# Kernel tuning notes

Measured on AMD Instinct MI355X. Metric: run time of the kernel, lower is better.

The kernel has to match this reference:

```python
import jax, jax.numpy as jnp
import numpy as np

N_NODES = 100000
N_EDGES = 1600000
IN_DIM = 128
HID = 128
EMB = 64


def _glorot(key, shape):
    fan_in, fan_out = shape[0], shape[1]
    lim = np.sqrt(6.0 / (fan_in + fan_out))
    return jax.random.uniform(key, shape, jnp.float32, -lim, lim)


def setup_inputs() -> dict:
    key = jax.random.key(0)
    ks = jax.random.split(key, 16)
    x = jax.random.normal(ks[0], (N_NODES, IN_DIM), jnp.float32)
    src = jax.random.randint(ks[1], (N_EDGES,), 0, N_NODES, jnp.int64)
    dst = jax.random.randint(ks[2], (N_EDGES,), 0, N_NODES, jnp.int64)
    # GCN encoder weights (GraphConv: weight [in,out], bias [out])
    W1 = _glorot(ks[3], (IN_DIM, HID)); b1 = jnp.zeros((HID,), jnp.float32)
    W2 = _glorot(ks[4], (HID, EMB)); b2 = jnp.zeros((EMB,), jnp.float32)
    # MLP predictor: 2*EMB=128 -> 64 -> 32 -> 1
    Wp1 = _glorot(ks[5], (2 * EMB, 64)); bp1 = jnp.zeros((64,), jnp.float32)
    Wp2 = _glorot(ks[6], (64, 32)); bp2 = jnp.zeros((32,), jnp.float32)
    Wp3 = _glorot(ks[7], (32, 1)); bp3 = jnp.zeros((1,), jnp.float32)
    return {"x": x, "src": src, "dst": dst,
            "W1": W1, "b1": b1, "W2": W2, "b2": b2,
            "Wp1": Wp1, "bp1": bp1, "Wp2": Wp2, "bp2": bp2,
            "Wp3": Wp3, "bp3": bp3}


def _gcn_conv(x, src, dst, W, b, n_nodes):
    # DGL GraphConv, norm='both': symmetric degree normalization, sum aggregation.
    ones = jnp.ones((src.shape[0],), x.dtype)
    deg_out = jnp.clip(jax.ops.segment_sum(ones, src, num_segments=n_nodes), 1.0)
    deg_in = jnp.clip(jax.ops.segment_sum(ones, dst, num_segments=n_nodes), 1.0)
    h = (x * jax.lax.rsqrt(deg_out)[:, None]) @ W          # [N, out]
    agg = jax.ops.segment_sum(h[src], dst, num_segments=n_nodes)  # gather + scatter-add
    return agg * jax.lax.rsqrt(deg_in)[:, None] + b


def reference(x, src, dst, W1, b1, W2, b2, Wp1, bp1, Wp2, bp2, Wp3, bp3):
    n = x.shape[0]
    h = jax.nn.relu(_gcn_conv(x, src, dst, W1, b1, n))   # layer 1 (with activation)
    h = _gcn_conv(h, src, dst, W2, b2, n)                # layer 2 (no activation)
    # edge-wise concat of endpoint embeddings: [E, 2*EMB]
    emb = jnp.concatenate([h[src], h[dst]], axis=1)
    z = jax.nn.relu(emb @ Wp1 + bp1)
    z = jax.nn.relu(z @ Wp2 + bp2)
    score = z @ Wp3 + bp3                                # [E, 1]
    return jax.nn.sigmoid(score)
```

## Files before the change

kernel.cpp:

```cpp
#include <hip/hip_runtime.h>
#include <math.h>


#define NBLK 256
#define NBUK 512
#define GRD (NBUK * NBLK)
#define GRT (2 * GRD)

typedef __attribute__((ext_vector_type(8))) short bf16x8;
typedef __attribute__((ext_vector_type(4))) float f32x4;

__device__ __forceinline__ float bl(unsigned u) { return __uint_as_float(u << 16); }
__device__ __forceinline__ float bh(unsigned u) { return __uint_as_float(u & 0xffff0000u); }
__device__ __forceinline__ unsigned short f2bf(float f) {
  unsigned u = __float_as_uint(f);
  return (unsigned short)((u + 0x7fffu + ((u >> 16) & 1u)) >> 16);
}
__device__ __forceinline__ unsigned packbf2(float a, float b) {
  return (unsigned)f2bf(a) | ((unsigned)f2bf(b) << 16);
}


__global__ __launch_bounds__(256) void k_hist(
    const int* __restrict__ src, const int* __restrict__ dst,
    int* __restrict__ grams, int E,
    const float* __restrict__ W1, const float* __restrict__ W2,
    const float* __restrict__ Wp1, const float* __restrict__ Wp2,
    unsigned short* __restrict__ W1t, unsigned short* __restrict__ W2t,
    unsigned short* __restrict__ Wct, unsigned short* __restrict__ Wp2t) {
  __shared__ int hd[NBUK], hs[NBUK];
  int blk = blockIdx.x, t = threadIdx.x;
  {
    int i = blk * 256 + t;
    if (i < 16384) {
      int n = i >> 7, k = i & 127;
      W1t[i] = f2bf(W1[k * 128 + n]);
    } else if (i < 24576) {
      int j = i - 16384; int n = j >> 7, k = j & 127;
      W2t[j] = f2bf(W2[k * 64 + n]);
    } else if (i < 32768) {
      int j = i - 24576; int c = j >> 6, k = j & 63;
      float v = (c < 64) ? Wp1[k * 64 + c] : Wp1[(k + 64) * 64 + (c - 64)];
      Wct[j] = f2bf(v);
    } else if (i < 34816) {
      int j = i - 32768; int n = j >> 6, k = j & 63;
      Wp2t[j] = f2bf(Wp2[k * 32 + n]);
    }
  }
  for (int k = t; k < NBUK; k += 256) { hd[k] = 0; hs[k] = 0; }
  __syncthreads();
  int chunk = (E + NBLK - 1) / NBLK;
  int start = blk * chunk, end = min(E, start + chunk);
  for (int i = start + t; i < end; i += 256) {
    atomicAdd(&hd[dst[i] >> 8], 1);
    atomicAdd(&hs[src[i] >> 8], 1);
  }
  __syncthreads();
  for (int k = t; k < NBUK; k += 256) {
    grams[k * NBLK + blk] = hd[k];
    grams[GRD + k * NBLK + blk] = hs[k];
  }
}

__global__ __launch_bounds__(256) void k_gscan1(const int* __restrict__ g,
                                                int* __restrict__ bsum) {
  __shared__ int lds[256];
  int b = blockIdx.x, t = threadIdx.x;
  int base = b * 1024 + t * 4;
  int s = g[base] + g[base + 1] + g[base + 2] + g[base + 3];
  lds[t] = s; __syncthreads();
  for (int st = 128; st > 0; st >>= 1) {
    if (t < st) lds[t] += lds[t + st];
    __syncthreads();
  }
  if (t == 0) bsum[b] = lds[0];
}

__global__ __launch_bounds__(256) void k_gscan3(int* __restrict__ g,
                                                const int* __restrict__ bsum) {
  __shared__ int lds[256], lds2[256];
  int b = blockIdx.x, t = threadIdx.x;
  int bv = bsum[t];
  lds2[t] = bv; __syncthreads();
  for (int st = 1; st < 256; st <<= 1) {
    int add = (t >= st) ? lds2[t - st] : 0;
    __syncthreads();
    lds2[t] += add;
    __syncthreads();
  }
  int bpref = (b > 0) ? lds2[b - 1] : 0;

  int base = b * 1024 + t * 4;
  int v[4]; int s = 0;
#pragma unroll
  for (int j = 0; j < 4; j++) { v[j] = g[base + j]; s += v[j]; }
  lds[t] = s; __syncthreads();
  int mine = s;
  for (int st = 1; st < 256; st <<= 1) {
    int add = (t >= st) ? lds[t - st] : 0;
    __syncthreads();
    lds[t] += add;
    __syncthreads();
  }
  int excl = lds[t] - mine + bpref;
#pragma unroll
  for (int j = 0; j < 4; j++) { g[base + j] = excl; excl += v[j]; }
}

__global__ __launch_bounds__(256) void k_part(
    const int* __restrict__ src, const int* __restrict__ dst,
    const int* __restrict__ grams, uint2* __restrict__ pdst,
    int* __restrict__ sbuf, int E) {
  __shared__ int curd[NBUK], curs[NBUK];
  int blk = blockIdx.x, t = threadIdx.x;
  for (int k = t; k < NBUK; k += 256) {
    curd[k] = grams[k * NBLK + blk];
    curs[k] = grams[GRD + k * NBLK + blk] - E;
  }
  __syncthreads();
  int chunk = (E + NBLK - 1) / NBLK;
  int start = blk * chunk, end = min(E, start + chunk);
  for (int i = start + t; i < end; i += 256) {
    int s = src[i], d = dst[i];
    int pd = atomicAdd(&curd[d >> 8], 1);
    pdst[pd] = make_uint2((unsigned)s, (unsigned)i | ((unsigned)(d & 255) << 21));
    int ps = atomicAdd(&curs[s >> 8], 1);
    sbuf[ps] = s;
  }
}

__global__ __launch_bounds__(256) void k_dcsr(
    const uint2* __restrict__ pdst, const int* __restrict__ sbuf,
    const int* __restrict__ grams,
    int* __restrict__ adj, int* __restrict__ dnode, int* __restrict__ eidx,
    int* __restrict__ rowst, float* __restrict__ rin, float* __restrict__ rout,
    int N, int E) {
  __shared__ int hist[256], cur[256];
  int b = blockIdx.x, t = threadIdx.x;
  int base = grams[b * 256];
  int end  = grams[b * 256 + 256];
  hist[t] = 0; __syncthreads();
  for (int i = base + t; i < end; i += 256)
    atomicAdd(&hist[(pdst[i].y >> 21) & 255], 1);
  __syncthreads();
  int cnt = hist[t];
  for (int st = 1; st < 256; st <<= 1) {
    int add = (t >= st) ? hist[t - st] : 0;
    __syncthreads();
    hist[t] += add;
    __syncthreads();
  }
  int excl = hist[t] - cnt;
  cur[t] = excl;
  int node = b * 256 + t;
  if (node < N) {
    rowst[node] = base + excl;
    rin[node] = rsqrtf((float)max(cnt, 1));
  }
  __syncthreads();
  for (int i = base + t; i < end; i += 256) {
    uint2 u = pdst[i];
    int lo = (u.y >> 21) & 255;
    int eid = (int)(u.y & 0x1FFFFFu);
    int pos = base + atomicAdd(&cur[lo], 1);
    adj[pos] = (int)u.x;
    dnode[pos] = b * 256 + lo;
    eidx[pos] = eid;
  }
  __syncthreads();
  hist[t] = 0; __syncthreads();
  int sb = grams[GRD + b * 256] - E;
  int se = grams[GRD + b * 256 + 256] - E;
  for (int i = sb + t; i < se; i += 256)
    atomicAdd(&hist[sbuf[i] & 255], 1);
  __syncthreads();
  if (node < N) rout[node] = rsqrtf((float)max(hist[t], 1));
}

template <int K, int BN, bool ABF, bool SC>
__global__ __launch_bounds__(256) void k_gemm(
    const void* __restrict__ Av, const float* __restrict__ scale,
    const unsigned short* __restrict__ Wt, unsigned short* __restrict__ C, int M) {
  constexpr int KP = K + 8;
  __shared__ __attribute__((aligned(16))) unsigned short As[64][KP];
  __shared__ __attribute__((aligned(16))) unsigned short Ws[BN][KP];
  int tid = threadIdx.x;
  int row0 = blockIdx.x * 64;

  for (int i = tid; i < BN * K / 8; i += 256) {
    int n = i / (K / 8), seg = i % (K / 8);
    *(uint4*)&Ws[n][seg * 8] = ((const uint4*)Wt)[i];
  }
  {
    constexpr int CH = K / 4;
    int r = tid >> 2, q = tid & 3;
    int row = row0 + r;
    if (row < M) {
      float sc = SC ? scale[row] : 1.0f;
      if constexpr (!ABF) {
        const float4* ap = (const float4*)((const float*)Av + (size_t)row * K + q * CH);
#pragma unroll
        for (int c = 0; c < CH / 8; c++) {
          float4 v0 = ap[2 * c], v1 = ap[2 * c + 1];
          uint4 o;
          o.x = packbf2(v0.x * sc, v0.y * sc);
          o.y = packbf2(v0.z * sc, v0.w * sc);
          o.z = packbf2(v1.x * sc, v1.y * sc);
          o.w = packbf2(v1.z * sc, v1.w * sc);
          *(uint4*)&As[r][q * CH + c * 8] = o;
        }
      } else {
        const uint4* ap = (const uint4*)((const unsigned short*)Av + (size_t)row * K + q * CH);
#pragma unroll
        for (int c = 0; c < CH / 8; c++) {
          uint4 v = ap[c];
          if constexpr (SC) {
            uint4 o;
            o.x = packbf2(bl(v.x) * sc, bh(v.x) * sc);
            o.y = packbf2(bl(v.y) * sc, bh(v.y) * sc);
            o.z = packbf2(bl(v.z) * sc, bh(v.z) * sc);
            o.w = packbf2(bl(v.w) * sc, bh(v.w) * sc);
            *(uint4*)&As[r][q * CH + c * 8] = o;
          } else {
            *(uint4*)&As[r][q * CH + c * 8] = v;
          }
        }
      }
    } else {
#pragma unroll
      for (int c = 0; c < CH / 8; c++)
        *(uint4*)&As[r][q * CH + c * 8] = make_uint4(0, 0, 0, 0);
    }
  }
  __syncthreads();

  constexpr int KS = K / 32;
  constexpr int NT = BN / 16;
  int wav = tid >> 6, lane = tid & 63;
  int quad = lane >> 4, lrow = lane & 15;
  int mb = wav * 16;

  bf16x8 af[KS];
#pragma unroll
  for (int s = 0; s < KS; s++)
    af[s] = *(const bf16x8*)&As[mb + lrow][s * 32 + quad * 8];

  f32x4 acc[NT];
#pragma unroll
  for (int nt = 0; nt < NT; nt++) acc[nt] = (f32x4){0.f, 0.f, 0.f, 0.f};
#pragma unroll
  for (int nt = 0; nt < NT; nt++) {
#pragma unroll
    for (int s = 0; s < KS; s++) {
      bf16x8 bf = *(const bf16x8*)&Ws[nt * 16 + lrow][s * 32 + quad * 8];
      acc[nt] = __builtin_amdgcn_mfma_f32_16x16x32_bf16(af[s], bf, acc[nt], 0, 0, 0);
    }
  }
#pragma unroll
  for (int nt = 0; nt < NT; nt++) {
#pragma unroll
    for (int reg = 0; reg < 4; reg++) {
      int row = row0 + mb + quad * 4 + reg;
      if (row < M) C[(size_t)row * BN + nt * 16 + lrow] = f2bf(acc[nt][reg]);
    }
  }
}

template <int F>
__global__ __launch_bounds__(256) void k_agg(
    const unsigned short* __restrict__ hin, const int* __restrict__ rowst,
    const int* __restrict__ adj, const float* __restrict__ rin,
    const float* __restrict__ bias, unsigned short* __restrict__ hout,
    int N, int E, int do_relu) {
  int node = (blockIdx.x * 256 + threadIdx.x) >> 6;
  int lane = threadIdx.x & 63;
  if (node >= N) return;
  int start = rowst[node];
  int end = (node + 1 < N) ? rowst[node + 1] : E;
  int half = lane >> 5, fl = lane & 31;
  if (F == 128) {
    const uint2* h2 = (const uint2*)hin;
    float a0 = 0.f, a1 = 0.f, a2 = 0.f, a3 = 0.f;
    float c0 = 0.f, c1 = 0.f, c2 = 0.f, c3 = 0.f;
    int i = start + half;
    for (; i + 2 < end; i += 4) {
      uint2 w0 = h2[(size_t)adj[i] * 32 + fl];
      uint2 w1 = h2[(size_t)adj[i + 2] * 32 + fl];
      a0 += bl(w0.x); a1 += bh(w0.x); a2 += bl(w0.y); a3 += bh(w0.y);
      c0 += bl(w1.x); c1 += bh(w1.x); c2 += bl(w1.y); c3 += bh(w1.y);
    }
    if (i < end) {
      uint2 w0 = h2[(size_t)adj[i] * 32 + fl];
      a0 += bl(w0.x); a1 += bh(w0.x); a2 += bl(w0.y); a3 += bh(w0.y);
    }
    a0 += c0; a1 += c1; a2 += c2; a3 += c3;
    a0 += __shfl_xor(a0, 32, 64);
    a1 += __shfl_xor(a1, 32, 64);
    a2 += __shfl_xor(a2, 32, 64);
    a3 += __shfl_xor(a3, 32, 64);
    float r = rin[node];
    float o0 = fmaf(a0, r, bias[fl * 4 + 0]);
    float o1 = fmaf(a1, r, bias[fl * 4 + 1]);
    float o2 = fmaf(a2, r, bias[fl * 4 + 2]);
    float o3 = fmaf(a3, r, bias[fl * 4 + 3]);
    if (do_relu) {
      o0 = fmaxf(o0, 0.f); o1 = fmaxf(o1, 0.f);
      o2 = fmaxf(o2, 0.f); o3 = fmaxf(o3, 0.f);
    }
    if (half == 0) {
      uint2 o; o.x = packbf2(o0, o1); o.y = packbf2(o2, o3);
      *(uint2*)((unsigned*)hout + (size_t)node * 64 + fl * 2) = o;
    }
  } else {
    const unsigned* h2 = (const unsigned*)hin;
    float a0 = 0.f, a1 = 0.f, c0 = 0.f, c1 = 0.f;
    int i = start + half;
    for (; i + 2 < end; i += 4) {
      unsigned w0 = h2[(size_t)adj[i] * 32 + fl];
      unsigned w1 = h2[(size_t)adj[i + 2] * 32 + fl];
      a0 += bl(w0); a1 += bh(w0);
      c0 += bl(w1); c1 += bh(w1);
    }
    if (i < end) {
      unsigned w0 = h2[(size_t)adj[i] * 32 + fl];
      a0 += bl(w0); a1 += bh(w0);
    }
    a0 += c0; a1 += c1;
    a0 += __shfl_xor(a0, 32, 64);
    a1 += __shfl_xor(a1, 32, 64);
    float r = rin[node];
    float o0 = fmaf(a0, r, bias[fl * 2 + 0]);
    float o1 = fmaf(a1, r, bias[fl * 2 + 1]);
    if (do_relu) { o0 = fmaxf(o0, 0.f); o1 = fmaxf(o1, 0.f); }
    if (half == 0)
      ((unsigned*)hout)[(size_t)node * 32 + fl] = packbf2(o0, o1);
  }
}

__global__ __launch_bounds__(256) void k_edge(
    const unsigned short* __restrict__ ab, const int* __restrict__ adj,
    const int* __restrict__ dnode, const int* __restrict__ eidx,
    const unsigned short* __restrict__ Wp2t, const float* __restrict__ bp1,
    const float* __restrict__ bp2, const float* __restrict__ Wp3,
    const float* __restrict__ bp3, float* __restrict__ out, int E) {
  __shared__ __attribute__((aligned(16))) unsigned short z1s[128][72];
  __shared__ __attribute__((aligned(16))) unsigned short w2t[32][72];
  __shared__ float sb1[64], sb2[32], sw3[32];

  int t = threadIdx.x;
  {
    uint4 v = ((const uint4*)Wp2t)[t];
    int n = t >> 3, seg = t & 7;
    *(uint4*)&w2t[n][seg * 8] = v;
    if (t < 64) sb1[t] = bp1[t];
    else if (t < 96) sb2[t - 64] = bp2[t - 64];
    else if (t < 128) sw3[t - 96] = Wp3[t - 96];
  }
  __syncthreads();

  int p0 = blockIdx.x * 128;
  {
    int m = t >> 1, half = t & 1, p = p0 + m;
    int s = 0, d = 0;
    if (p < E) { s = adj[p]; d = dnode[p]; }
    const uint4* apf = (const uint4*)(ab + (size_t)s * 128 + half * 32);
    const uint4* bpf = (const uint4*)(ab + (size_t)d * 128 + 64 + half * 32);
    int jb = half * 32;
#pragma unroll
    for (int q = 0; q < 4; q++) {
      uint4 av = apf[q], bv = bpf[q];
      int j = jb + 8 * q;
      float z0 = fmaxf(bl(av.x) + bl(bv.x) + sb1[j + 0], 0.f);
      float z1 = fmaxf(bh(av.x) + bh(bv.x) + sb1[j + 1], 0.f);
      float z2 = fmaxf(bl(av.y) + bl(bv.y) + sb1[j + 2], 0.f);
      float z3 = fmaxf(bh(av.y) + bh(bv.y) + sb1[j + 3], 0.f);
      float z4 = fmaxf(bl(av.z) + bl(bv.z) + sb1[j + 4], 0.f);
      float z5 = fmaxf(bh(av.z) + bh(bv.z) + sb1[j + 5], 0.f);
      float z6 = fmaxf(bl(av.w) + bl(bv.w) + sb1[j + 6], 0.f);
      float z7 = fmaxf(bh(av.w) + bh(bv.w) + sb1[j + 7], 0.f);
      uint4 o;
      o.x = packbf2(z0, z1); o.y = packbf2(z2, z3);
      o.z = packbf2(z4, z5); o.w = packbf2(z6, z7);
      *(uint4*)&z1s[m][j] = o;
    }
  }
  __syncthreads();

  int wav = t >> 6, lane = t & 63;
  int quad = lane >> 4, lrow = lane & 15;

  bf16x8 bfr[2][2];
#pragma unroll
  for (int s = 0; s < 2; s++)
#pragma unroll
    for (int nt = 0; nt < 2; nt++)
      bfr[s][nt] = *(const bf16x8*)&w2t[nt * 16 + lrow][s * 32 + quad * 8];

  f32x4 acc[2][2];
#pragma unroll
  for (int mt = 0; mt < 2; mt++)
#pragma unroll
    for (int nt = 0; nt < 2; nt++) acc[mt][nt] = (f32x4){0.f, 0.f, 0.f, 0.f};

#pragma unroll
  for (int mt = 0; mt < 2; mt++) {
    int mb = (wav * 2 + mt) * 16;
#pragma unroll
    for (int s = 0; s < 2; s++) {
      bf16x8 a = *(const bf16x8*)&z1s[mb + lrow][s * 32 + quad * 8];
#pragma unroll
      for (int nt = 0; nt < 2; nt++)
        acc[mt][nt] = __builtin_amdgcn_mfma_f32_16x16x32_bf16(a, bfr[s][nt], acc[mt][nt], 0, 0, 0);
    }
  }

  float bb0 = sb2[lrow], bb1 = sb2[16 + lrow];
  float w30 = sw3[lrow], w31 = sw3[16 + lrow];
  float p2[2][4];
#pragma unroll
  for (int mt = 0; mt < 2; mt++)
#pragma unroll
    for (int reg = 0; reg < 4; reg++)
      p2[mt][reg] = fmaxf(acc[mt][0][reg] + bb0, 0.f) * w30 +
                    fmaxf(acc[mt][1][reg] + bb1, 0.f) * w31;
#pragma unroll
  for (int off = 1; off < 16; off <<= 1) {
#pragma unroll
    for (int mt = 0; mt < 2; mt++)
#pragma unroll
      for (int reg = 0; reg < 4; reg++)
        p2[mt][reg] += __shfl_xor(p2[mt][reg], off, 64);
  }
  if (lrow < 4) {
    float b3 = bp3[0];
#pragma unroll
    for (int mt = 0; mt < 2; mt++) {
      float score = p2[mt][0];
      if (lrow == 1) score = p2[mt][1];
      if (lrow == 2) score = p2[mt][2];
      if (lrow == 3) score = p2[mt][3];
      score += b3;
      int pp = p0 + (wav * 2 + mt) * 16 + quad * 4 + lrow;
      if (pp < E) out[eidx[pp]] = 1.0f / (1.0f + __expf(-score));
    }
  }
}

extern "C" void kernel_launch(void* const* d_in, const int* in_sizes, int n_in,
                              void* d_out, int out_size, void* d_ws, size_t ws_size,
                              hipStream_t stream) {
  const float* x   = (const float*)d_in[0];
  const int*   src = (const int*)d_in[1];
  const int*   dst = (const int*)d_in[2];
  const float* W1  = (const float*)d_in[3];
  const float* b1  = (const float*)d_in[4];
  const float* W2  = (const float*)d_in[5];
  const float* b2  = (const float*)d_in[6];
  const float* Wp1 = (const float*)d_in[7];
  const float* bp1 = (const float*)d_in[8];
  const float* Wp2 = (const float*)d_in[9];
  const float* bp2 = (const float*)d_in[10];
  const float* Wp3 = (const float*)d_in[11];
  const float* bp3 = (const float*)d_in[12];
  float* out = (float*)d_out;

  int N = in_sizes[0] / 128;
  int E = in_sizes[1];

  char* w = (char*)d_ws;
  unsigned short* bufA = (unsigned short*)w;
  uint2* pdst = (uint2*)w;
  int*   sbuf = (int*)(w + (size_t)E * 8);
  w += (size_t)N * 128 * 2;
  unsigned short* bufB = (unsigned short*)w; w += (size_t)N * 128 * 2;
  int* grams  = (int*)w;    w += (size_t)GRT * sizeof(int);
  int* bsum   = (int*)w;    w += 256 * sizeof(int);
  int* rowst  = (int*)w;    w += (size_t)N * sizeof(int);
  int* adj    = (int*)w;    w += (size_t)E * sizeof(int);
  int* dnode  = (int*)w;    w += (size_t)E * sizeof(int);
  int* eidx   = (int*)w;    w += (size_t)E * sizeof(int);
  float* rin  = (float*)w;  w += (size_t)N * sizeof(float);
  float* rout = (float*)w;  w += (size_t)N * sizeof(float);
  unsigned short* W1t  = (unsigned short*)w; w += 16384 * 2;
  unsigned short* W2t  = (unsigned short*)w; w += 8192 * 2;
  unsigned short* Wct  = (unsigned short*)w; w += 8192 * 2;
  unsigned short* Wp2t = (unsigned short*)w; w += 2048 * 2;

  int nbk = (N + 255) / 256;

  k_hist<<<NBLK, 256, 0, stream>>>(src, dst, grams, E, W1, W2, Wp1, Wp2,
                                   W1t, W2t, Wct, Wp2t);
  k_gscan1<<<GRT / 1024, 256, 0, stream>>>(grams, bsum);
  k_gscan3<<<GRT / 1024, 256, 0, stream>>>(grams, bsum);
  k_part<<<NBLK, 256, 0, stream>>>(src, dst, grams, pdst, sbuf, E);
  k_dcsr<<<nbk, 256, 0, stream>>>(pdst, sbuf, grams, adj, dnode, eidx,
                                  rowst, rin, rout, N, E);

  k_gemm<128, 128, false, true><<<(N + 63) / 64, 256, 0, stream>>>(x, rout, W1t, bufA, N);
  k_agg<128><<<(N + 3) / 4, 256, 0, stream>>>(bufA, rowst, adj, rin, b1, bufB, N, E, 1);
  k_gemm<128, 64, true, true><<<(N + 63) / 64, 256, 0, stream>>>(bufB, rout, W2t, bufA, N);
  k_agg<64><<<(N + 3) / 4, 256, 0, stream>>>(bufA, rowst, adj, rin, b2, bufB, N, E, 0);
  k_gemm<64, 128, true, false><<<(N + 63) / 64, 256, 0, stream>>>(bufB, nullptr, Wct, bufA, N);
  k_edge<<<(E + 127) / 128, 256, 0, stream>>>(bufA, adj, dnode, eidx, Wp2t,
                                              bp1, bp2, Wp3, bp3, out, E);
}
```

Baseline: 433.3 us.

## Compact CSR build, process edges in original order, widen agg gather to 16B

The partition buffer is packed from 8 bytes to 4 bytes per edge, and the source histogram buffer now stores a single low byte. The dnode and eidx arrays are dropped, so the edge MLP reads src and dst directly in original order and writes output without a scatter. The aggregation kernel now gives each thread 16-byte vector loads, with 16 or 8 threads per node and four neighbors unrolled per step, replacing half-wave splitting and shuffles. This cuts memory traffic in CSR construction and the edge stage, at the cost of losing the dst-sorted locality the edge kernel previously had when gathering embeddings.

```diff
diff --git a/kernel.cpp b/kernel.cpp
--- a/kernel.cpp
+++ b/kernel.cpp
@@ -109,8 +109,8 @@
 
 __global__ __launch_bounds__(256) void k_part(
     const int* __restrict__ src, const int* __restrict__ dst,
-    const int* __restrict__ grams, uint2* __restrict__ pdst,
-    int* __restrict__ sbuf, int E) {
+    const int* __restrict__ grams, unsigned* __restrict__ pdst,
+    unsigned char* __restrict__ sbuf, int E) {
   __shared__ int curd[NBUK], curs[NBUK];
   int blk = blockIdx.x, t = threadIdx.x;
   for (int k = t; k < NBUK; k += 256) {
@@ -123,25 +123,24 @@
   for (int i = start + t; i < end; i += 256) {
     int s = src[i], d = dst[i];
     int pd = atomicAdd(&curd[d >> 8], 1);
-    pdst[pd] = make_uint2((unsigned)s, (unsigned)i | ((unsigned)(d & 255) << 21));
+    pdst[pd] = ((unsigned)s << 8) | (unsigned)(d & 255);
     int ps = atomicAdd(&curs[s >> 8], 1);
-    sbuf[ps] = s;
+    sbuf[ps] = (unsigned char)(s & 255);
   }
 }
 
 __global__ __launch_bounds__(256) void k_dcsr(
-    const uint2* __restrict__ pdst, const int* __restrict__ sbuf,
+    const unsigned* __restrict__ pdst, const unsigned char* __restrict__ sbuf,
     const int* __restrict__ grams,
-    int* __restrict__ adj, int* __restrict__ dnode, int* __restrict__ eidx,
-    int* __restrict__ rowst, float* __restrict__ rin, float* __restrict__ rout,
-    int N, int E) {
+    int* __restrict__ adj, int* __restrict__ rowst,
+    float* __restrict__ rin, float* __restrict__ rout, int N, int E) {
   __shared__ int hist[256], cur[256];
   int b = blockIdx.x, t = threadIdx.x;
   int base = grams[b * 256];
   int end  = grams[b * 256 + 256];
   hist[t] = 0; __syncthreads();
   for (int i = base + t; i < end; i += 256)
-    atomicAdd(&hist[(pdst[i].y >> 21) & 255], 1);
+    atomicAdd(&hist[pdst[i] & 255], 1);
   __syncthreads();
   int cnt = hist[t];
   for (int st = 1; st < 256; st <<= 1) {
@@ -159,20 +158,16 @@
   }
   __syncthreads();
   for (int i = base + t; i < end; i += 256) {
-    uint2 u = pdst[i];
-    int lo = (u.y >> 21) & 255;
-    int eid = (int)(u.y & 0x1FFFFFu);
-    int pos = base + atomicAdd(&cur[lo], 1);
-    adj[pos] = (int)u.x;
-    dnode[pos] = b * 256 + lo;
-    eidx[pos] = eid;
+    unsigned u = pdst[i];
+    int pos = base + atomicAdd(&cur[u & 255], 1);
+    adj[pos] = (int)(u >> 8);
   }
   __syncthreads();
   hist[t] = 0; __syncthreads();
   int sb = grams[GRD + b * 256] - E;
   int se = grams[GRD + b * 256 + 256] - E;
   for (int i = sb + t; i < se; i += 256)
-    atomicAdd(&hist[sbuf[i] & 255], 1);
+    atomicAdd(&hist[sbuf[i]], 1);
   __syncthreads();
   if (node < N) rout[node] = rsqrtf((float)max(hist[t], 1));
 }
@@ -272,74 +267,64 @@
     const int* __restrict__ adj, const float* __restrict__ rin,
     const float* __restrict__ bias, unsigned short* __restrict__ hout,
     int N, int E, int do_relu) {
-  int node = (blockIdx.x * 256 + threadIdx.x) >> 6;
-  int lane = threadIdx.x & 63;
+  constexpr int TPN = F / 8;
+  constexpr int NPB = 256 / TPN;
+  int node = blockIdx.x * NPB + threadIdx.x / TPN;
+  int c = threadIdx.x % TPN;
   if (node >= N) return;
   int start = rowst[node];
   int end = (node + 1 < N) ? rowst[node + 1] : E;
-  int half = lane >> 5, fl = lane & 31;
-  if (F == 128) {
-    const uint2* h2 = (const uint2*)hin;
-    float a0 = 0.f, a1 = 0.f, a2 = 0.f, a3 = 0.f;
-    float c0 = 0.f, c1 = 0.f, c2 = 0.f, c3 = 0.f;
-    int i = start + half;
-    for (; i + 2 < end; i += 4) {
-      uint2 w0 = h2[(size_t)adj[i] * 32 + fl];
-      uint2 w1 = h2[(size_t)adj[i + 2] * 32 + fl];
-      a0 += bl(w0.x); a1 += bh(w0.x); a2 += bl(w0.y); a3 += bh(w0.y);
-      c0 += bl(w1.x); c1 += bh(w1.x); c2 += bl(w1.y); c3 += bh(w1.y);
-    }
-    if (i < end) {
-      uint2 w0 = h2[(size_t)adj[i] * 32 + fl];
-      a0 += bl(w0.x); a1 += bh(w0.x); a2 += bl(w0.y); a3 += bh(w0.y);
-    }
-    a0 += c0; a1 += c1; a2 += c2; a3 += c3;
-    a0 += __shfl_xor(a0, 32, 64);
-    a1 += __shfl_xor(a1, 32, 64);
-    a2 += __shfl_xor(a2, 32, 64);
-    a3 += __shfl_xor(a3, 32, 64);
-    float r = rin[node];
-    float o0 = fmaf(a0, r, bias[fl * 4 + 0]);
-    float o1 = fmaf(a1, r, bias[fl * 4 + 1]);
-    float o2 = fmaf(a2, r, bias[fl * 4 + 2]);
-    float o3 = fmaf(a3, r, bias[fl * 4 + 3]);
-    if (do_relu) {
-      o0 = fmaxf(o0, 0.f); o1 = fmaxf(o1, 0.f);
-      o2 = fmaxf(o2, 0.f); o3 = fmaxf(o3, 0.f);
-    }
-    if (half == 0) {
-      uint2 o; o.x = packbf2(o0, o1); o.y = packbf2(o2, o3);
-      *(uint2*)((unsigned*)hout + (size_t)node * 64 + fl * 2) = o;
-    }
-  } else {
-    const unsigned* h2 = (const unsigned*)hin;
-    float a0 = 0.f, a1 = 0.f, c0 = 0.f, c1 = 0.f;
-    int i = start + half;
-    for (; i + 2 < end; i += 4) {
-      unsigned w0 = h2[(size_t)adj[i] * 32 + fl];
-      unsigned w1 = h2[(size_t)adj[i + 2] * 32 + fl];
-      a0 += bl(w0); a1 += bh(w0);
-      c0 += bl(w1); c1 += bh(w1);
-    }
-    if (i < end) {
-      unsigned w0 = h2[(size_t)adj[i] * 32 + fl];
-      a0 += bl(w0); a1 += bh(w0);
-    }
-    a0 += c0; a1 += c1;
-    a0 += __shfl_xor(a0, 32, 64);
-    a1 += __shfl_xor(a1, 32, 64);
-    float r = rin[node];
-    float o0 = fmaf(a0, r, bias[fl * 2 + 0]);
-    float o1 = fmaf(a1, r, bias[fl * 2 + 1]);
-    if (do_relu) { o0 = fmaxf(o0, 0.f); o1 = fmaxf(o1, 0.f); }
-    if (half == 0)
-      ((unsigned*)hout)[(size_t)node * 32 + fl] = packbf2(o0, o1);
-  }
+  const uint4* h4 = (const uint4*)hin;
+
+  float a[8], b[8];
+#pragma unroll
+  for (int j = 0; j < 8; j++) { a[j] = 0.f; b[j] = 0.f; }
+
+  int i = start;
+  for (; i + 3 < end; i += 4) {
+    uint4 w0 = h4[(size_t)adj[i] * TPN + c];
+    uint4 w1 = h4[(size_t)adj[i + 1] * TPN + c];
+    uint4 w2 = h4[(size_t)adj[i + 2] * TPN + c];
+    uint4 w3 = h4[(size_t)adj[i + 3] * TPN + c];
+    a[0] += bl(w0.x); a[1] += bh(w0.x); a[2] += bl(w0.y); a[3] += bh(w0.y);
+    a[4] += bl(w0.z); a[5] += bh(w0.z); a[6] += bl(w0.w); a[7] += bh(w0.w);
+    b[0] += bl(w1.x); b[1] += bh(w1.x); b[2] += bl(w1.y); b[3] += bh(w1.y);
+    b[4] += bl(w1.z); b[5] += bh(w1.z); b[6] += bl(w1.w); b[7] += bh(w1.w);
+    a[0] += bl(w2.x); a[1] += bh(w2.x); a[2] += bl(w2.y); a[3] += bh(w2.y);
+    a[4] += bl(w2.z); a[5] += bh(w2.z); a[6] += bl(w2.w); a[7] += bh(w2.w);
+    b[0] += bl(w3.x); b[1] += bh(w3.x); b[2] += bl(w3.y); b[3] += bh(w3.y);
+    b[4] += bl(w3.z); b[5] += bh(w3.z); b[6] += bl(w3.w); b[7] += bh(w3.w);
+  }
+  for (; i < end; i++) {
+    uint4 w0 = h4[(size_t)adj[i] * TPN + c];
+    a[0] += bl(w0.x); a[1] += bh(w0.x); a[2] += bl(w0.y); a[3] += bh(w0.y);
+    a[4] += bl(w0.z); a[5] += bh(w0.z); a[6] += bl(w0.w); a[7] += bh(w0.w);
+  }
+  float r = rin[node];
+  const float4* bp = (const float4*)(bias + c * 8);
+  float4 bb0 = bp[0], bb1 = bp[1];
+  float o0 = fmaf(a[0] + b[0], r, bb0.x);
+  float o1 = fmaf(a[1] + b[1], r, bb0.y);
+  float o2 = fmaf(a[2] + b[2], r, bb0.z);
+  float o3 = fmaf(a[3] + b[3], r, bb0.w);
+  float o4 = fmaf(a[4] + b[4], r, bb1.x);
+  float o5 = fmaf(a[5] + b[5], r, bb1.y);
+  float o6 = fmaf(a[6] + b[6], r, bb1.z);
+  float o7 = fmaf(a[7] + b[7], r, bb1.w);
+  if (do_relu) {
+    o0 = fmaxf(o0, 0.f); o1 = fmaxf(o1, 0.f); o2 = fmaxf(o2, 0.f);
+    o3 = fmaxf(o3, 0.f); o4 = fmaxf(o4, 0.f); o5 = fmaxf(o5, 0.f);
+    o6 = fmaxf(o6, 0.f); o7 = fmaxf(o7, 0.f);
+  }
+  uint4 o;
+  o.x = packbf2(o0, o1); o.y = packbf2(o2, o3);
+  o.z = packbf2(o4, o5); o.w = packbf2(o6, o7);
+  ((uint4*)hout)[(size_t)node * TPN + c] = o;
 }
 
 __global__ __launch_bounds__(256) void k_edge(
-    const unsigned short* __restrict__ ab, const int* __restrict__ adj,
-    const int* __restrict__ dnode, const int* __restrict__ eidx,
+    const unsigned short* __restrict__ ab, const int* __restrict__ src,
+    const int* __restrict__ dst,
     const unsigned short* __restrict__ Wp2t, const float* __restrict__ bp1,
     const float* __restrict__ bp2, const float* __restrict__ Wp3,
     const float* __restrict__ bp3, float* __restrict__ out, int E) {
@@ -362,7 +347,7 @@
   {
     int m = t >> 1, half = t & 1, p = p0 + m;
     int s = 0, d = 0;
-    if (p < E) { s = adj[p]; d = dnode[p]; }
+    if (p < E) { s = src[p]; d = dst[p]; }
     const uint4* apf = (const uint4*)(ab + (size_t)s * 128 + half * 32);
     const uint4* bpf = (const uint4*)(ab + (size_t)d * 128 + 64 + half * 32);
     int jb = half * 32;
@@ -441,7 +426,7 @@
       if (lrow == 3) score = p2[mt][3];
       score += b3;
       int pp = p0 + (wav * 2 + mt) * 16 + quad * 4 + lrow;
-      if (pp < E) out[eidx[pp]] = 1.0f / (1.0f + __expf(-score));
+      if (pp < E) out[pp] = 1.0f / (1.0f + __expf(-score));
     }
   }
 }
@@ -469,16 +454,14 @@
 
   char* w = (char*)d_ws;
   unsigned short* bufA = (unsigned short*)w;
-  uint2* pdst = (uint2*)w;
-  int*   sbuf = (int*)(w + (size_t)E * 8);
+  unsigned* pdst = (unsigned*)w;
+  unsigned char* sbuf = (unsigned char*)(w + (size_t)E * 4);
   w += (size_t)N * 128 * 2;
   unsigned short* bufB = (unsigned short*)w; w += (size_t)N * 128 * 2;
   int* grams  = (int*)w;    w += (size_t)GRT * sizeof(int);
   int* bsum   = (int*)w;    w += 256 * sizeof(int);
   int* rowst  = (int*)w;    w += (size_t)N * sizeof(int);
   int* adj    = (int*)w;    w += (size_t)E * sizeof(int);
-  int* dnode  = (int*)w;    w += (size_t)E * sizeof(int);
-  int* eidx   = (int*)w;    w += (size_t)E * sizeof(int);
   float* rin  = (float*)w;  w += (size_t)N * sizeof(float);
   float* rout = (float*)w;  w += (size_t)N * sizeof(float);
   unsigned short* W1t  = (unsigned short*)w; w += 16384 * 2;
@@ -493,14 +476,13 @@
   k_gscan1<<<GRT / 1024, 256, 0, stream>>>(grams, bsum);
   k_gscan3<<<GRT / 1024, 256, 0, stream>>>(grams, bsum);
   k_part<<<NBLK, 256, 0, stream>>>(src, dst, grams, pdst, sbuf, E);
-  k_dcsr<<<nbk, 256, 0, stream>>>(pdst, sbuf, grams, adj, dnode, eidx,
-                                  rowst, rin, rout, N, E);
+  k_dcsr<<<nbk, 256, 0, stream>>>(pdst, sbuf, grams, adj, rowst, rin, rout, N, E);
 
   k_gemm<128, 128, false, true><<<(N + 63) / 64, 256, 0, stream>>>(x, rout, W1t, bufA, N);
-  k_agg<128><<<(N + 3) / 4, 256, 0, stream>>>(bufA, rowst, adj, rin, b1, bufB, N, E, 1);
+  k_agg<128><<<(N + 15) / 16, 256, 0, stream>>>(bufA, rowst, adj, rin, b1, bufB, N, E, 1);
   k_gemm<128, 64, true, true><<<(N + 63) / 64, 256, 0, stream>>>(bufB, rout, W2t, bufA, N);
-  k_agg<64><<<(N + 3) / 4, 256, 0, stream>>>(bufA, rowst, adj, rin, b2, bufB, N, E, 0);
+  k_agg<64><<<(N + 31) / 32, 256, 0, stream>>>(bufA, rowst, adj, rin, b2, bufB, N, E, 0);
   k_gemm<64, 128, true, false><<<(N + 63) / 64, 256, 0, stream>>>(bufB, nullptr, Wct, bufA, N);
-  k_edge<<<(E + 127) / 128, 256, 0, stream>>>(bufA, adj, dnode, eidx, Wp2t,
+  k_edge<<<(E + 127) / 128, 256, 0, stream>>>(bufA, src, dst, Wp2t,
                                               bp1, bp2, Wp3, bp3, out, E);
 }
```

Result: faster. 378.5 us (-12.6%).
